# Optimization experiments

Measured on AMD Instinct MI355X. Metric: run time of the kernel, lower is better.

The kernel has to match this reference:

```python
import jax, jax.numpy as jnp
from jax import lax
import numpy as np

B, T, I, H, C = 32, 256, 128, 128, 100


def setup_inputs() -> dict:
    key = jax.random.key(0)
    ks = jax.random.split(key, 9)
    s = 1.0 / np.sqrt(H)  # PyTorch LSTMCell init range
    inp = {
        "x": jax.random.normal(ks[0], (B, T, I), dtype=jnp.float32),
        "w_ih": jax.random.uniform(ks[1], (4 * H, I), jnp.float32, -s, s),
        "b_ih": jax.random.uniform(ks[2], (4 * H,), jnp.float32, -s, s),
        "w_hh": jax.random.uniform(ks[3], (4 * H, H), jnp.float32, -s, s),
        "b_hh": jax.random.uniform(ks[4], (4 * H,), jnp.float32, -s, s),
        # attention params: normal(mean=0, std=0.01) per the source
        "w1": 0.01 * jax.random.normal(ks[5], (2 * H, H), dtype=jnp.float32),
        "w2": 0.01 * jax.random.normal(ks[6], (H, 1), dtype=jnp.float32),
        "w_fc": jax.random.uniform(ks[7], (C, H), jnp.float32, -s, s),
        "b_fc": jax.random.uniform(ks[8], (C,), jnp.float32, -s, s),
    }
    return inp


def _forward(x, w_ih, b_ih, w_hh, b_hh, w1, w2, w_fc, b_fc):
    Bv, Tv, _ = x.shape
    Hv = w_hh.shape[1]
    h0 = jnp.zeros((Bv, Hv), x.dtype)
    c0 = jnp.zeros((Bv, Hv), x.dtype)
    # memory buffer: slot 0 holds the initial zero hidden state (as in the
    # torch code, h_old starts as h_t=0); slots 1..T filled as we go.
    # Unwritten (future) slots are zero, so their attn contribution
    # attn_w * h_old is exactly zero -> no mask needed, matching the
    # growing-memory semantics of the original loop.
    mem0 = jnp.zeros((Bv, Tv + 1, Hv), x.dtype)
    attn0 = jnp.zeros((Bv, Hv), x.dtype)

    def step(carry, inp):
        h, c, mem, _ = carry
        x_t, i = inp
        # PyTorch LSTMCell: gate order i, f, g, o
        gates = x_t @ w_ih.T + b_ih + h @ w_hh.T + b_hh
        ig, fg, gg, og = jnp.split(gates, 4, axis=-1)
        c = jax.nn.sigmoid(fg) * c + jax.nn.sigmoid(ig) * jnp.tanh(gg)
        h = jax.nn.sigmoid(og) * jnp.tanh(c)
        # additive attention scores over the memory (NO softmax in source)
        h_rep = jnp.broadcast_to(h[:, None, :], mem.shape)  # [B, T+1, H]
        cat = jnp.concatenate([h_rep, mem], axis=-1)        # [B, T+1, 2H]
        s = jnp.tanh(cat @ w1) @ w2                          # [B, T+1, 1]
        attn_c = jnp.sum(s * mem, axis=1)                    # [B, H]
        mem = mem.at[:, i + 1, :].set(h)  # append h_t to memory
        return (h, c, mem, attn_c), None

    xs = (jnp.transpose(x, (1, 0, 2)), jnp.arange(Tv))
    (h, c, mem, attn_c), _ = lax.scan(step, (h0, c0, mem0, attn0), xs)
    return (h + attn_c) @ w_fc.T + b_fc


def reference(x, w_ih, b_ih, w_hh, b_hh, w1, w2, w_fc, b_fc):
    return _forward(x, w_ih, b_ih, w_hh, b_hh, w1, w2, w_fc, b_fc)
```

## Files before the change

### kernel.cpp

```cpp
#include <hip/hip_runtime.h>
#include <hip/hip_bf16.h>


#define Bsz 32
#define Tsz 256
#define Isz 128
#define Hsz 128
#define Csz 100
#define G4H 512

__device__ __forceinline__ float2 pk_fma(float2 a, float2 b, float2 c) {
    float2 d;
    asm("v_pk_fma_f32 %0, %1, %2, %3" : "=v"(d) : "v"(a), "v"(b), "v"(c));
    return d;
}
__device__ __forceinline__ float quad_rsum(float x) {
    int t = __builtin_amdgcn_update_dpp(0, __float_as_int(x), 0xB1, 0xF, 0xF, true);
    x += __int_as_float(t);
    t = __builtin_amdgcn_update_dpp(0, __float_as_int(x), 0x4E, 0xF, 0xF, true);
    x += __int_as_float(t);
    return x;
}
__device__ __forceinline__ float rcpf(float x) { return __builtin_amdgcn_rcpf(x); }
__device__ __forceinline__ float sigm_n(float x) { return rcpf(1.0f + __expf(-x)); }
__device__ __forceinline__ float tanh_n(float x) {
    float ax = fabsf(x);
    float e = __expf(-2.0f * ax);
    float t = (1.0f - e) * rcpf(1.0f + e);
    return copysignf(t, x);
}
__device__ __forceinline__ float tanh_s(float x) { return tanh_n(x); }

__global__ __launch_bounds__(256) void prep_kernel(
    const float* __restrict__ w_ih, const float* __restrict__ b_ih,
    const float* __restrict__ w_hh, const float* __restrict__ b_hh,
    float* __restrict__ wih_t, float* __restrict__ whh_pk, float* __restrict__ bias) {
    int idx = blockIdx.x * blockDim.x + threadIdx.x;
    if (idx < G4H * Isz) {
        int j = idx >> 7;
        int k = idx & 127;
        wih_t[k * G4H + j] = w_ih[idx];

        int j4  = idx & 3;
        int q   = (idx >> 2) & 3;
        int d   = (idx >> 4) & 127;
        int gi  = (idx >> 11) & 3;
        int kk4 = (idx >> 13) & 7;
        whh_pk[idx] = w_hh[(size_t)((gi << 7) + d) * 128 + (q << 5) + (kk4 << 2) + j4];
    }
    if (idx < G4H) bias[idx] = b_ih[idx] + b_hh[idx];
}

#define GBK 16
#define GLD 132

__global__ __launch_bounds__(256) void gemm128(
    const float* __restrict__ A, const float* __restrict__ Bm,
    const float* __restrict__ bias, float* __restrict__ C,
    int M, int N, int K) {
    __shared__ float As[GBK][GLD];
    __shared__ float Bs[GBK][GLD];
    const int tid = threadIdx.x;
    const int bm = blockIdx.y * 128;
    const int bn = blockIdx.x * 128;
    const int tx = tid & 15, ty = tid >> 4;
    float acc[8][8] = {};

    const int ar = tid >> 2;
    const int ac = (tid & 3) * 4;
    const int br = tid >> 5;
    const int bc = (tid & 31) * 4;

    for (int k0 = 0; k0 < K; k0 += GBK) {
        #pragma unroll
        for (int h = 0; h < 2; ++h) {
            int r = ar + 64 * h;
            float4 v = *(const float4*)(A + (size_t)(bm + r) * K + k0 + ac);
            As[ac + 0][r] = v.x;
            As[ac + 1][r] = v.y;
            As[ac + 2][r] = v.z;
            As[ac + 3][r] = v.w;
        }
        #pragma unroll
        for (int h = 0; h < 2; ++h) {
            int kr = br + 8 * h;
            float4 v = *(const float4*)(Bm + (size_t)(k0 + kr) * N + bn + bc);
            *(float4*)&Bs[kr][bc] = v;
        }
        __syncthreads();
        #pragma unroll
        for (int kk = 0; kk < GBK; ++kk) {
            float a[8], b[8];
            *(float4*)&a[0] = *(const float4*)&As[kk][ty * 8];
            *(float4*)&a[4] = *(const float4*)&As[kk][ty * 8 + 4];
            *(float4*)&b[0] = *(const float4*)&Bs[kk][tx * 8];
            *(float4*)&b[4] = *(const float4*)&Bs[kk][tx * 8 + 4];
            #pragma unroll
            for (int i = 0; i < 8; ++i)
                #pragma unroll
                for (int j = 0; j < 8; ++j)
                    acc[i][j] = fmaf(a[i], b[j], acc[i][j]);
        }
        __syncthreads();
    }
    float bb[8];
    #pragma unroll
    for (int j = 0; j < 8; ++j) bb[j] = bias ? bias[bn + tx * 8 + j] : 0.0f;
    #pragma unroll
    for (int i = 0; i < 8; ++i) {
        int row = bm + ty * 8 + i;
        float4 v0, v1;
        v0.x = acc[i][0] + bb[0]; v0.y = acc[i][1] + bb[1];
        v0.z = acc[i][2] + bb[2]; v0.w = acc[i][3] + bb[3];
        v1.x = acc[i][4] + bb[4]; v1.y = acc[i][5] + bb[5];
        v1.z = acc[i][6] + bb[6]; v1.w = acc[i][7] + bb[7];
        *(float4*)(C + (size_t)row * N + bn + tx * 8) = v0;
        *(float4*)(C + (size_t)row * N + bn + tx * 8 + 4) = v1;
    }
}

#define HPAD(k) ((k) + 8 * ((k) >> 5))

__global__ __launch_bounds__(512, 2) void lstm_seq(
    const float* __restrict__ G, const float* __restrict__ whh_pk,
    float* __restrict__ H_all) {
    const int b = blockIdx.x;
    const int tid = threadIdx.x;
    const int d = tid >> 2;
    const int q = tid & 3;

    __shared__ float h_s[2][160];

    float2 w2v[4][16];
    {
        const float4* wp = (const float4*)whh_pk;
        #pragma unroll
        for (int kk4 = 0; kk4 < 8; ++kk4)
            #pragma unroll
            for (int gi = 0; gi < 4; ++gi) {
                float4 v = wp[((kk4 * 4 + gi) * 128 + d) * 4 + q];
                w2v[gi][kk4 * 2]     = make_float2(v.x, v.y);
                w2v[gi][kk4 * 2 + 1] = make_float2(v.z, v.w);
            }
    }

    if (tid < 320) ((float*)h_s)[tid] = 0.0f;
    float c = 0.0f;
    __syncthreads();

    const float* Gq = G + (size_t)b * Tsz * G4H + q * 128 + d;
    float* Hst = H_all + (size_t)b * Tsz * Hsz + d;

    float hring[8];
    int cur = 0;

    for (int t0 = 0; t0 < Tsz; t0 += 8) {
        float gb[8];
        #pragma unroll
        for (int s = 0; s < 8; ++s) gb[s] = Gq[(size_t)(t0 + s) * G4H];
        if (t0 > 0 && q == 0) {
            #pragma unroll
            for (int s = 0; s < 8; ++s) Hst[(size_t)(t0 - 8 + s) * Hsz] = hring[s];
        }

        #pragma unroll
        for (int ph = 0; ph < 8; ++ph) {
            float gval = gb[ph];
            float2 accA[4], accB[4];
            #pragma unroll
            for (int gi = 0; gi < 4; ++gi) {
                accA[gi] = make_float2(q == gi ? gval : 0.f, 0.f);
                accB[gi] = make_float2(0.f, 0.f);
            }
            const float4* hb4 = (const float4*)&h_s[cur][q * 40];
            #pragma unroll
            for (int kk4 = 0; kk4 < 8; ++kk4) {
                float4 h4 = hb4[kk4];
                float2 hA = make_float2(h4.x, h4.y);
                float2 hB = make_float2(h4.z, h4.w);
                accA[0] = pk_fma(hA, w2v[0][2 * kk4], accA[0]);
                accA[1] = pk_fma(hA, w2v[1][2 * kk4], accA[1]);
                accA[2] = pk_fma(hA, w2v[2][2 * kk4], accA[2]);
                accA[3] = pk_fma(hA, w2v[3][2 * kk4], accA[3]);
                accB[0] = pk_fma(hB, w2v[0][2 * kk4 + 1], accB[0]);
                accB[1] = pk_fma(hB, w2v[1][2 * kk4 + 1], accB[1]);
                accB[2] = pk_fma(hB, w2v[2][2 * kk4 + 1], accB[2]);
                accB[3] = pk_fma(hB, w2v[3][2 * kk4 + 1], accB[3]);
            }
            float a0 = quad_rsum(accA[0].x + accA[0].y + accB[0].x + accB[0].y);
            float a1 = quad_rsum(accA[1].x + accA[1].y + accB[1].x + accB[1].y);
            float a2 = quad_rsum(accA[2].x + accA[2].y + accB[2].x + accB[2].y);
            float a3 = quad_rsum(accA[3].x + accA[3].y + accB[3].x + accB[3].y);

            float iv = sigm_n(a0);
            float fv = sigm_n(a1);
            float gv = tanh_n(a2);
            float ov = sigm_n(a3);
            c = fv * c + iv * gv;
            float h = ov * tanh_n(c);

            if (q == 0) h_s[cur ^ 1][HPAD(d)] = h;
            hring[ph] = h;
            __syncthreads();
            cur ^= 1;
        }
    }
    if (q == 0) {
        #pragma unroll
        for (int s = 0; s < 8; ++s) Hst[(size_t)(248 + s) * Hsz] = hring[s];
    }
}

__global__ __launch_bounds__(256) void attn_out(
    const float* __restrict__ H_all, const float* __restrict__ KV,
    const float* __restrict__ w1, const float* __restrict__ w2,
    const float* __restrict__ w_fc, const float* __restrict__ b_fc,
    float* __restrict__ out) {
    int b = blockIdx.x;
    int tid = threadIdx.x;
    __shared__ float hT[Hsz];
    __shared__ float q_s[Hsz];
    __shared__ float w2s[Hsz];
    __shared__ float s_s[Tsz];
    __shared__ float r2[2][Hsz];
    __shared__ float r_s[Hsz];

    const float* Hb = H_all + (size_t)b * Tsz * Hsz;
    const float* KVb = KV + (size_t)b * Tsz * Hsz;

    if (tid < Hsz) {
        hT[tid] = Hb[255 * Hsz + tid];
        w2s[tid] = w2[tid];
    }
    __syncthreads();
    if (tid < Hsz) {
        float acc = 0.f;
        #pragma unroll 8
        for (int k = 0; k < Hsz; ++k) acc = fmaf(hT[k], w1[k * Hsz + tid], acc);
        q_s[tid] = acc;
    }
    __syncthreads();

    const int qd = tid >> 2, ql = tid & 3;
    #pragma unroll
    for (int jj = 0; jj < 4; ++jj) {
        int j = qd + jj * 64;
        float p = 0.f;
        if (j < 255) {
            const float* kv = KVb + (size_t)j * Hsz + ql * 32;
            const float* qs = q_s + ql * 32;
            const float* wv = w2s + ql * 32;
            #pragma unroll 8
            for (int k = 0; k < 32; ++k)
                p = fmaf(tanh_s(qs[k] + kv[k]), wv[k], p);
        }
        p = quad_rsum(p);
        if (ql == 0 && j < 255) s_s[j] = p;
    }
    __syncthreads();

    {
        int dd = tid & 127, half = tid >> 7;
        int j0 = half * 128, je = half ? 255 : 128;
        float acc = 0.f;
        #pragma unroll 4
        for (int j = j0; j < je; ++j) acc = fmaf(s_s[j], Hb[(size_t)j * Hsz + dd], acc);
        r2[half][dd] = acc;
    }
    __syncthreads();
    if (tid < Hsz) r_s[tid] = hT[tid] + r2[0][tid] + r2[1][tid];
    __syncthreads();

    {
        int o = tid >> 1, half = tid & 1;
        float acc = 0.f;
        if (o < Csz) {
            const float* wr = w_fc + (size_t)o * Hsz + half * 64;
            const float* rr = r_s + half * 64;
            #pragma unroll 8
            for (int k = 0; k < 64; ++k) acc = fmaf(rr[k], wr[k], acc);
        }
        acc += __shfl_xor(acc, 1);
        if (half == 0 && o < Csz) out[b * Csz + o] = acc + b_fc[o];
    }
}

extern "C" void kernel_launch(void* const* d_in, const int* in_sizes, int n_in,
                              void* d_out, int out_size, void* d_ws, size_t ws_size,
                              hipStream_t stream) {
    const float* x    = (const float*)d_in[0];
    const float* w_ih = (const float*)d_in[1];
    const float* b_ih = (const float*)d_in[2];
    const float* w_hh = (const float*)d_in[3];
    const float* b_hh = (const float*)d_in[4];
    const float* w1   = (const float*)d_in[5];
    const float* w2   = (const float*)d_in[6];
    const float* w_fc = (const float*)d_in[7];
    const float* b_fc = (const float*)d_in[8];

    float* ws = (float*)d_ws;
    float* wih_t  = ws;
    float* whh_pk = wih_t + 65536;
    float* bias   = whh_pk + 65536;
    float* G      = bias + 512;
    float* H_all  = G + 4194304;
    float* KV     = H_all + 1048576;

    prep_kernel<<<256, 256, 0, stream>>>(w_ih, b_ih, w_hh, b_hh, wih_t, whh_pk, bias);

    dim3 g1(G4H / 128, (Bsz * Tsz) / 128);
    gemm128<<<g1, 256, 0, stream>>>(x, wih_t, bias, G, Bsz * Tsz, G4H, Isz);

    lstm_seq<<<Bsz, 512, 0, stream>>>(G, whh_pk, H_all);

    dim3 g2(Hsz / 128, (Bsz * Tsz) / 128);
    gemm128<<<g2, 256, 0, stream>>>(H_all, w1 + Hsz * Hsz, nullptr, KV, Bsz * Tsz, Hsz, Hsz);

    attn_out<<<Bsz, 256, 0, stream>>>(H_all, KV, w1, w2, w_fc, b_fc, (float*)d_out);
}
```

Baseline: 341.1 us.

## Replace FP32 GEMMs with split-bf16 MFMA GEMMs and simplify LSTM store loop

Replaces the two SIMT fp32 GEMMs (input projection and key projection) with an MFMA bf16 GEMM that uses a hi/lo split of both operands (three products: hi*hi, lo*hi, hi*lo) to approximate fp32 accuracy. This adds split kernels that convert x and H_all to bf16 pairs, and preprocessing of the w_ih and w1 weights into the split layout. The LSTM recurrence also drops its 8-step batching of gate loads and h stores, prefetching one step ahead and storing h every step instead. The intent is to cut GEMM time with matrix cores, at the cost of extra conversion passes and slightly reduced precision.

```diff
diff --git a/kernel.cpp b/kernel.cpp
--- a/kernel.cpp
+++ b/kernel.cpp
@@ -8,6 +8,9 @@
 #define Hsz 128
 #define Csz 100
 #define G4H 512
+
+typedef short v8s __attribute__((ext_vector_type(8)));
+typedef float v4fa __attribute__((ext_vector_type(4)));
 
 __device__ __forceinline__ float2 pk_fma(float2 a, float2 b, float2 c) {
     float2 d;
@@ -34,12 +37,19 @@
 __global__ __launch_bounds__(256) void prep_kernel(
     const float* __restrict__ w_ih, const float* __restrict__ b_ih,
     const float* __restrict__ w_hh, const float* __restrict__ b_hh,
-    float* __restrict__ wih_t, float* __restrict__ whh_pk, float* __restrict__ bias) {
+    const float* __restrict__ w1,
+    __hip_bfloat16* __restrict__ W2ih, __hip_bfloat16* __restrict__ W2v,
+    float* __restrict__ whh_pk, float* __restrict__ bias) {
     int idx = blockIdx.x * blockDim.x + threadIdx.x;
     if (idx < G4H * Isz) {
-        int j = idx >> 7;
+        int n = idx >> 7;
         int k = idx & 127;
-        wih_t[k * G4H + j] = w_ih[idx];
+        float x = w_ih[idx];
+        __hip_bfloat16 hi = __float2bfloat16(x);
+        __hip_bfloat16 lo = __float2bfloat16(x - __bfloat162float(hi));
+        W2ih[(size_t)n * 384 + k] = hi;
+        W2ih[(size_t)n * 384 + 128 + k] = lo;
+        W2ih[(size_t)n * 384 + 256 + k] = hi;
 
         int j4  = idx & 3;
         int q   = (idx >> 2) & 3;
@@ -48,75 +58,68 @@
         int kk4 = (idx >> 13) & 7;
         whh_pk[idx] = w_hh[(size_t)((gi << 7) + d) * 128 + (q << 5) + (kk4 << 2) + j4];
     }
+    if (idx < Hsz * Hsz) {
+        int n = idx >> 7;
+        int k = idx & 127;
+        float x = w1[(size_t)(128 + k) * Hsz + n];
+        __hip_bfloat16 hi = __float2bfloat16(x);
+        __hip_bfloat16 lo = __float2bfloat16(x - __bfloat162float(hi));
+        W2v[(size_t)n * 384 + k] = hi;
+        W2v[(size_t)n * 384 + 128 + k] = lo;
+        W2v[(size_t)n * 384 + 256 + k] = hi;
+    }
     if (idx < G4H) bias[idx] = b_ih[idx] + b_hh[idx];
 }
 
-#define GBK 16
-#define GLD 132
-
-__global__ __launch_bounds__(256) void gemm128(
-    const float* __restrict__ A, const float* __restrict__ Bm,
-    const float* __restrict__ bias, float* __restrict__ C,
-    int M, int N, int K) {
-    __shared__ float As[GBK][GLD];
-    __shared__ float Bs[GBK][GLD];
+__global__ __launch_bounds__(256) void split256(
+    const float* __restrict__ src, __hip_bfloat16* __restrict__ dst, int total) {
+    int i = blockIdx.x * 256 + threadIdx.x;
+    if (i >= total) return;
+    int m = i >> 7, k = i & 127;
+    float x = src[i];
+    __hip_bfloat16 hi = __float2bfloat16(x);
+    dst[(size_t)m * 256 + k] = hi;
+    dst[(size_t)m * 256 + 128 + k] = __float2bfloat16(x - __bfloat162float(hi));
+}
+
+__global__ __launch_bounds__(256) void gemm_mfma(
+    const __hip_bfloat16* __restrict__ A2, const __hip_bfloat16* __restrict__ W2,
+    const float* __restrict__ bias, float* __restrict__ C, int M, int N) {
     const int tid = threadIdx.x;
-    const int bm = blockIdx.y * 128;
-    const int bn = blockIdx.x * 128;
-    const int tx = tid & 15, ty = tid >> 4;
-    float acc[8][8] = {};
-
-    const int ar = tid >> 2;
-    const int ac = (tid & 3) * 4;
-    const int br = tid >> 5;
-    const int bc = (tid & 31) * 4;
-
-    for (int k0 = 0; k0 < K; k0 += GBK) {
+    const int w = tid >> 6, lane = tid & 63;
+    const int m0 = blockIdx.y * 64 + (w & 1) * 32;
+    const int n0 = blockIdx.x * 64 + (w >> 1) * 32;
+    const int r = lane & 15, quad = lane >> 4;
+
+    v4fa acc[2][2] = {};
+    const short* Ab = (const short*)A2;
+    const short* Wb = (const short*)W2;
+
+    #pragma unroll
+    for (int ks = 0; ks < 12; ++ks) {
+        int ka = (ks & 3) * 32 + ((ks >= 8) ? 128 : 0) + quad * 8;
+        int kb = ks * 32 + quad * 8;
+        v8s a0 = *(const v8s*)(Ab + (size_t)(m0 + r) * 256 + ka);
+        v8s a1 = *(const v8s*)(Ab + (size_t)(m0 + 16 + r) * 256 + ka);
+        v8s b0 = *(const v8s*)(Wb + (size_t)(n0 + r) * 384 + kb);
+        v8s b1 = *(const v8s*)(Wb + (size_t)(n0 + 16 + r) * 384 + kb);
+        acc[0][0] = __builtin_amdgcn_mfma_f32_16x16x32_bf16(a0, b0, acc[0][0], 0, 0, 0);
+        acc[0][1] = __builtin_amdgcn_mfma_f32_16x16x32_bf16(a0, b1, acc[0][1], 0, 0, 0);
+        acc[1][0] = __builtin_amdgcn_mfma_f32_16x16x32_bf16(a1, b0, acc[1][0], 0, 0, 0);
+        acc[1][1] = __builtin_amdgcn_mfma_f32_16x16x32_bf16(a1, b1, acc[1][1], 0, 0, 0);
+    }
+    #pragma unroll
+    for (int i = 0; i < 2; ++i)
         #pragma unroll
-        for (int h = 0; h < 2; ++h) {
-            int r = ar + 64 * h;
-            float4 v = *(const float4*)(A + (size_t)(bm + r) * K + k0 + ac);
-            As[ac + 0][r] = v.x;
-            As[ac + 1][r] = v.y;
-            As[ac + 2][r] = v.z;
-            As[ac + 3][r] = v.w;
-        }
-        #pragma unroll
-        for (int h = 0; h < 2; ++h) {
-            int kr = br + 8 * h;
-            float4 v = *(const float4*)(Bm + (size_t)(k0 + kr) * N + bn + bc);
-            *(float4*)&Bs[kr][bc] = v;
-        }
-        __syncthreads();
-        #pragma unroll
-        for (int kk = 0; kk < GBK; ++kk) {
-            float a[8], b[8];
-            *(float4*)&a[0] = *(const float4*)&As[kk][ty * 8];
-            *(float4*)&a[4] = *(const float4*)&As[kk][ty * 8 + 4];
-            *(float4*)&b[0] = *(const float4*)&Bs[kk][tx * 8];
-            *(float4*)&b[4] = *(const float4*)&Bs[kk][tx * 8 + 4];
+        for (int j = 0; j < 2; ++j) {
+            int cn = n0 + 16 * j + r;
+            float bb = bias ? bias[cn] : 0.0f;
             #pragma unroll
-            for (int i = 0; i < 8; ++i)
-                #pragma unroll
-                for (int j = 0; j < 8; ++j)
-                    acc[i][j] = fmaf(a[i], b[j], acc[i][j]);
-        }
-        __syncthreads();
-    }
-    float bb[8];
-    #pragma unroll
-    for (int j = 0; j < 8; ++j) bb[j] = bias ? bias[bn + tx * 8 + j] : 0.0f;
-    #pragma unroll
-    for (int i = 0; i < 8; ++i) {
-        int row = bm + ty * 8 + i;
-        float4 v0, v1;
-        v0.x = acc[i][0] + bb[0]; v0.y = acc[i][1] + bb[1];
-        v0.z = acc[i][2] + bb[2]; v0.w = acc[i][3] + bb[3];
-        v1.x = acc[i][4] + bb[4]; v1.y = acc[i][5] + bb[5];
-        v1.z = acc[i][6] + bb[6]; v1.w = acc[i][7] + bb[7];
-        *(float4*)(C + (size_t)row * N + bn + tx * 8) = v0;
-        *(float4*)(C + (size_t)row * N + bn + tx * 8 + 4) = v1;
-    }
+            for (int rr = 0; rr < 4; ++rr) {
+                int row = m0 + 16 * i + quad * 4 + rr;
+                C[(size_t)row * N + cn] = acc[i][j][rr] + bb;
+            }
+        }
 }
 
 #define HPAD(k) ((k) + 8 * ((k) >> 5))
@@ -151,63 +154,52 @@
     const float* Gq = G + (size_t)b * Tsz * G4H + q * 128 + d;
     float* Hst = H_all + (size_t)b * Tsz * Hsz + d;
 
-    float hring[8];
+    float gval = Gq[0];
     int cur = 0;
-
-    for (int t0 = 0; t0 < Tsz; t0 += 8) {
-        float gb[8];
+    for (int t = 0; t < Tsz; ++t) {
+        const int tn = (t < Tsz - 1) ? t + 1 : t;
+        float ngval = Gq[(size_t)tn * G4H];
+
+        float2 accA[4], accB[4];
         #pragma unroll
-        for (int s = 0; s < 8; ++s) gb[s] = Gq[(size_t)(t0 + s) * G4H];
-        if (t0 > 0 && q == 0) {
-            #pragma unroll
-            for (int s = 0; s < 8; ++s) Hst[(size_t)(t0 - 8 + s) * Hsz] = hring[s];
-        }
-
+        for (int gi = 0; gi < 4; ++gi) {
+            accA[gi] = make_float2(q == gi ? gval : 0.f, 0.f);
+            accB[gi] = make_float2(0.f, 0.f);
+        }
+        const float4* hb4 = (const float4*)&h_s[cur][q * 40];
         #pragma unroll
-        for (int ph = 0; ph < 8; ++ph) {
-            float gval = gb[ph];
-            float2 accA[4], accB[4];
-            #pragma unroll
-            for (int gi = 0; gi < 4; ++gi) {
-                accA[gi] = make_float2(q == gi ? gval : 0.f, 0.f);
-                accB[gi] = make_float2(0.f, 0.f);
-            }
-            const float4* hb4 = (const float4*)&h_s[cur][q * 40];
-            #pragma unroll
-            for (int kk4 = 0; kk4 < 8; ++kk4) {
-                float4 h4 = hb4[kk4];
-                float2 hA = make_float2(h4.x, h4.y);
-                float2 hB = make_float2(h4.z, h4.w);
-                accA[0] = pk_fma(hA, w2v[0][2 * kk4], accA[0]);
-                accA[1] = pk_fma(hA, w2v[1][2 * kk4], accA[1]);
-                accA[2] = pk_fma(hA, w2v[2][2 * kk4], accA[2]);
-                accA[3] = pk_fma(hA, w2v[3][2 * kk4], accA[3]);
-                accB[0] = pk_fma(hB, w2v[0][2 * kk4 + 1], accB[0]);
-                accB[1] = pk_fma(hB, w2v[1][2 * kk4 + 1], accB[1]);
-                accB[2] = pk_fma(hB, w2v[2][2 * kk4 + 1], accB[2]);
-                accB[3] = pk_fma(hB, w2v[3][2 * kk4 + 1], accB[3]);
-            }
-            float a0 = quad_rsum(accA[0].x + accA[0].y + accB[0].x + accB[0].y);
-            float a1 = quad_rsum(accA[1].x + accA[1].y + accB[1].x + accB[1].y);
-            float a2 = quad_rsum(accA[2].x + accA[2].y + accB[2].x + accB[2].y);
-            float a3 = quad_rsum(accA[3].x + accA[3].y + accB[3].x + accB[3].y);
-
-            float iv = sigm_n(a0);
-            float fv = sigm_n(a1);
-            float gv = tanh_n(a2);
-            float ov = sigm_n(a3);
-            c = fv * c + iv * gv;
-            float h = ov * tanh_n(c);
-
-            if (q == 0) h_s[cur ^ 1][HPAD(d)] = h;
-            hring[ph] = h;
-            __syncthreads();
-            cur ^= 1;
-        }
-    }
-    if (q == 0) {
-        #pragma unroll
-        for (int s = 0; s < 8; ++s) Hst[(size_t)(248 + s) * Hsz] = hring[s];
+        for (int kk4 = 0; kk4 < 8; ++kk4) {
+            float4 h4 = hb4[kk4];
+            float2 hA = make_float2(h4.x, h4.y);
+            float2 hB = make_float2(h4.z, h4.w);
+            accA[0] = pk_fma(hA, w2v[0][2 * kk4], accA[0]);
+            accA[1] = pk_fma(hA, w2v[1][2 * kk4], accA[1]);
+            accA[2] = pk_fma(hA, w2v[2][2 * kk4], accA[2]);
+            accA[3] = pk_fma(hA, w2v[3][2 * kk4], accA[3]);
+            accB[0] = pk_fma(hB, w2v[0][2 * kk4 + 1], accB[0]);
+            accB[1] = pk_fma(hB, w2v[1][2 * kk4 + 1], accB[1]);
+            accB[2] = pk_fma(hB, w2v[2][2 * kk4 + 1], accB[2]);
+            accB[3] = pk_fma(hB, w2v[3][2 * kk4 + 1], accB[3]);
+        }
+        float a0 = quad_rsum(accA[0].x + accA[0].y + accB[0].x + accB[0].y);
+        float a1 = quad_rsum(accA[1].x + accA[1].y + accB[1].x + accB[1].y);
+        float a2 = quad_rsum(accA[2].x + accA[2].y + accB[2].x + accB[2].y);
+        float a3 = quad_rsum(accA[3].x + accA[3].y + accB[3].x + accB[3].y);
+
+        float iv = sigm_n(a0);
+        float fv = sigm_n(a1);
+        float gv = tanh_n(a2);
+        float ov = sigm_n(a3);
+        c = fv * c + iv * gv;
+        float h = ov * tanh_n(c);
+
+        if (q == 0) {
+            h_s[cur ^ 1][HPAD(d)] = h;
+            Hst[(size_t)t * Hsz] = h;
+        }
+        gval = ngval;
+        __syncthreads();
+        cur ^= 1;
     }
 }
 
@@ -299,22 +291,30 @@
     const float* b_fc = (const float*)d_in[8];
 
     float* ws = (float*)d_ws;
-    float* wih_t  = ws;
-    float* whh_pk = wih_t + 65536;
+    float* whh_pk = ws;
     float* bias   = whh_pk + 65536;
-    float* G      = bias + 512;
+    __hip_bfloat16* W2ih = (__hip_bfloat16*)(bias + 512);
+    __hip_bfloat16* W2v  = (__hip_bfloat16*)(bias + 512 + 98304);
+    __hip_bfloat16* x2   = (__hip_bfloat16*)(bias + 512 + 98304 + 24576);
+    float* G      = bias + 512 + 98304 + 24576 + 1048576;
+    __hip_bfloat16* H2 = (__hip_bfloat16*)G;
+    float* KV     = G + 2097152;
     float* H_all  = G + 4194304;
-    float* KV     = H_all + 1048576;
-
-    prep_kernel<<<256, 256, 0, stream>>>(w_ih, b_ih, w_hh, b_hh, wih_t, whh_pk, bias);
-
-    dim3 g1(G4H / 128, (Bsz * Tsz) / 128);
-    gemm128<<<g1, 256, 0, stream>>>(x, wih_t, bias, G, Bsz * Tsz, G4H, Isz);
+
+    prep_kernel<<<256, 256, 0, stream>>>(w_ih, b_ih, w_hh, b_hh, w1,
+                                         W2ih, W2v, whh_pk, bias);
+
+    split256<<<4096, 256, 0, stream>>>(x, x2, Bsz * Tsz * Isz);
+
+    dim3 gG(G4H / 64, (Bsz * Tsz) / 64);
+    gemm_mfma<<<gG, 256, 0, stream>>>(x2, W2ih, bias, G, Bsz * Tsz, G4H);
 
     lstm_seq<<<Bsz, 512, 0, stream>>>(G, whh_pk, H_all);
 
-    dim3 g2(Hsz / 128, (Bsz * Tsz) / 128);
-    gemm128<<<g2, 256, 0, stream>>>(H_all, w1 + Hsz * Hsz, nullptr, KV, Bsz * Tsz, Hsz, Hsz);
+    split256<<<4096, 256, 0, stream>>>(H_all, H2, Bsz * Tsz * Hsz);
+
+    dim3 gK(Hsz / 64, (Bsz * Tsz) / 64);
+    gemm_mfma<<<gK, 256, 0, stream>>>(H2, W2v, nullptr, KV, Bsz * Tsz, Hsz);
 
     attn_out<<<Bsz, 256, 0, stream>>>(H_all, KV, w1, w2, w_fc, b_fc, (float*)d_out);
 }
```

After: 340.8 us. No clear change (-0.1%).
